# Kernel tuning notes

Hardware: AMD Instinct MI355X
Metric: run time of the kernel (lower is better)

Reference implementation:

```python
import math
import jax, jax.numpy as jnp
import numpy as np

VOCAB = 30522
HIDDEN = 768
TYPE_VOCAB = 2
EPS = 1e-12
MAX_LEN = 5000


def sin_table(dim, max_len=MAX_LEN):
    pos = jnp.arange(max_len, dtype=jnp.float32)[:, None]
    div = jnp.exp(jnp.arange(0, dim, 2, dtype=jnp.float32) * (-(math.log(10000.0) / dim)))
    ang = pos * div  # [max_len, dim//2]
    pe = jnp.zeros((max_len, dim), dtype=jnp.float32)
    pe = pe.at[:, 0::2].set(jnp.sin(ang))
    pe = pe.at[:, 1::2].set(jnp.cos(ang))
    return pe


def setup_inputs() -> dict:
    key = jax.random.key(0)
    k1, k2, k3, k4, k5, k6, k7 = jax.random.split(key, 7)
    B, S = 8, 4096
    input_ids = jax.random.randint(k1, (B, S), 0, VOCAB, dtype=jnp.int64 if jax.config.jax_enable_x64 else jnp.int32)
    tok_struct_vec = jax.random.randint(k2, (B, S, 3), 0, S, dtype=input_ids.dtype)
    sent_struct_vec = jax.random.randint(k3, (B, 64, 2), 0, 64, dtype=input_ids.dtype)
    token_type_ids = jax.random.randint(k4, (B, S), 0, TYPE_VOCAB, dtype=input_ids.dtype)
    word_emb = jax.random.normal(k5, (VOCAB, HIDDEN), dtype=jnp.float32) * 0.02
    word_emb = word_emb.at[0].set(0.0)  # padding_idx=0
    type_emb = jax.random.normal(k6, (TYPE_VOCAB, HIDDEN), dtype=jnp.float32) * 0.02
    ln_w = jnp.ones((HIDDEN,), dtype=jnp.float32)
    ln_b = jnp.zeros((HIDDEN,), dtype=jnp.float32)
    return {"input_ids": input_ids, "tok_struct_vec": tok_struct_vec,
            "sent_struct_vec": sent_struct_vec, "token_type_ids": token_type_ids,
            "word_emb": word_emb, "type_emb": type_emb, "ln_w": ln_w, "ln_b": ln_b}


def reference(input_ids, tok_struct_vec, sent_struct_vec, token_type_ids,
              word_emb, type_emb, ln_w, ln_b):
    B, S = input_ids.shape
    pe = sin_table(HIDDEN)[:S]            # [S, H]
    hs_pe = sin_table(HIDDEN // 3)[:S]    # [S, H/3]

    words = word_emb[input_ids]           # [B,S,H]
    tt = type_emb[token_type_ids]         # [B,S,H]

    # NOTE: faithful to source bug: compute_se closes over para_pos, so all
    # three struct embeddings gather with para_pos (tok_struct_vec[:,:,0]).
    para_pos = tok_struct_vec[:, :, 0]
    g = hs_pe[para_pos]                   # [B,S,H/3]
    struct = jnp.concatenate((g, g, g), axis=2)  # [B,S,H]

    emb = words + pe[None, :, :] + tt + struct
    mu = jnp.mean(emb, axis=-1, keepdims=True)
    var = jnp.mean(jnp.square(emb - mu), axis=-1, keepdims=True)
    out = (emb - mu) / jnp.sqrt(var + EPS) * ln_w + ln_b
    return out  # dropout is identity in eval mode
```

## Files before the change

### kernel.cpp

```cpp
#include <hip/hip_runtime.h>
#include <math.h>

#define HIDDEN 768

#define K768 (-0.011992630692677323f)
#define K256 (-0.035977892078031970f)
#define C256 (0.04641588833612779f)
#define C512 (0.002154434690031884f)

typedef float nfloat4 __attribute__((ext_vector_type(4)));

__global__ __launch_bounds__(256) void emb_ln_kernel(
    const int*   __restrict__ input_ids,
    const int*   __restrict__ tok_struct,
    const int*   __restrict__ token_type,
    const float* __restrict__ word_emb,
    const float* __restrict__ type_emb,
    const float* __restrict__ ln_w,
    const float* __restrict__ ln_b,
    float*       __restrict__ out,
    int S, int BS)
{
    const int wave = threadIdx.x >> 6;
    const int lane = threadIdx.x & 63;
    const int gw   = blockIdx.x * 4 + wave;
    const int NW   = gridDim.x * 4;

    const int h0 = lane * 4;

    const float d0 = __expf((float)h0 * K256);
    const float d1 = __expf((float)(h0 + 2) * K256);
    const float e0 = __expf((float)h0 * K768);
    const float e2 = __expf((float)(h0 + 2) * K768);

    float4 g[3], bb[3], t0[3], t1[3];
    const float4* wv = (const float4*)ln_w;
    const float4* bv = (const float4*)ln_b;
    const float4* te = (const float4*)type_emb;
#pragma unroll
    for (int j = 0; j < 3; ++j) {
        g[j]  = wv[lane + 64 * j];
        bb[j] = bv[lane + 64 * j];
        t0[j] = te[lane + 64 * j];
        t1[j] = te[lane + 64 * j + 192];
    }

    int r = gw;
    if (r >= BS) return;

    int id = input_ids[r];
    int tt = token_type[r];
    int pp = tok_struct[3 * r];
    float4 w[3];
    {
        const float4* wrow = (const float4*)(word_emb + (size_t)id * HIDDEN);
#pragma unroll
        for (int j = 0; j < 3; ++j) w[j] = wrow[lane + 64 * j];
    }

    while (true) {
        const int rn = r + NW;
        const bool has_next = rn < BS;

        int idn = 0, ttn = 0, ppn = 0;
        float4 wn[3];
        if (has_next) {
            idn = input_ids[rn];
            ttn = token_type[rn];
            ppn = tok_struct[3 * rn];
            const float4* wrow = (const float4*)(word_emb + (size_t)idn * HIDDEN);
#pragma unroll
            for (int j = 0; j < 3; ++j) wn[j] = wrow[lane + 64 * j];
        }

        const float fpp = (float)pp;
        float hs[4];
        hs[0] = __sinf(fpp * d0);
        hs[1] = __cosf(fpp * d0);
        hs[2] = __sinf(fpp * d1);
        hs[3] = __cosf(fpp * d1);

        const float fs = (float)(r & (S - 1));

        float v[12];
#pragma unroll
        for (int j = 0; j < 3; ++j) {
            const float scale = (j == 0) ? 1.0f : (j == 1 ? C256 : C512);
            const float a0 = fs * (e0 * scale);
            const float a1 = fs * (e2 * scale);
            const float4 ty = tt ? t1[j] : t0[j];
            v[4 * j + 0] = w[j].x + ty.x + __sinf(a0) + hs[0];
            v[4 * j + 1] = w[j].y + ty.y + __cosf(a0) + hs[1];
            v[4 * j + 2] = w[j].z + ty.z + __sinf(a1) + hs[2];
            v[4 * j + 3] = w[j].w + ty.w + __cosf(a1) + hs[3];
        }

        float s1 = 0.0f, s2 = 0.0f;
#pragma unroll
        for (int i = 0; i < 12; ++i) {
            s1 += v[i];
            s2 = fmaf(v[i], v[i], s2);
        }
#pragma unroll
        for (int off = 1; off < 64; off <<= 1) {
            s1 += __shfl_xor(s1, off, 64);
            s2 += __shfl_xor(s2, off, 64);
        }

        const float inv_n = 1.0f / (float)HIDDEN;
        const float mu = s1 * inv_n;
        const float rstd = rsqrtf(fmaxf(s2 * inv_n - mu * mu, 0.0f) + 1e-12f);

        nfloat4* orow = (nfloat4*)(out + (size_t)r * HIDDEN);
#pragma unroll
        for (int j = 0; j < 3; ++j) {
            nfloat4 rr;
            rr.x = (v[4 * j + 0] - mu) * rstd * g[j].x + bb[j].x;
            rr.y = (v[4 * j + 1] - mu) * rstd * g[j].y + bb[j].y;
            rr.z = (v[4 * j + 2] - mu) * rstd * g[j].z + bb[j].z;
            rr.w = (v[4 * j + 3] - mu) * rstd * g[j].w + bb[j].w;
            __builtin_nontemporal_store(rr, &orow[lane + 64 * j]);
        }

        if (!has_next) break;
        id = idn; tt = ttn; pp = ppn;
        w[0] = wn[0]; w[1] = wn[1]; w[2] = wn[2];
        r = rn;
    }
}

extern "C" void kernel_launch(void* const* d_in, const int* in_sizes, int n_in,
                              void* d_out, int out_size, void* d_ws, size_t ws_size,
                              hipStream_t stream) {
    const int*   input_ids  = (const int*)  d_in[0];
    const int*   tok_struct = (const int*)  d_in[1];
    const int*   token_type = (const int*)  d_in[3];
    const float* word_emb   = (const float*)d_in[4];
    const float* type_emb   = (const float*)d_in[5];
    const float* ln_w       = (const float*)d_in[6];
    const float* ln_b       = (const float*)d_in[7];
    float* out = (float*)d_out;

    const int BS = in_sizes[0];
    const int B  = in_sizes[2] / 128;
    const int S  = BS / B;

    int blocks = 2048;
    if (blocks * 4 > BS) blocks = (BS + 3) / 4;
    emb_ln_kernel<<<blocks, 256, 0, stream>>>(input_ids, tok_struct, token_type,
                                              word_emb, type_emb, ln_w, ln_b,
                                              out, S, BS);
}
```

Measured before the change: 188.5 us.

## Batch four rows per wave with all gathers issued upfront

Each wave now handles a fixed ROWS=4 rows. It first loads all ids and then issues every word-embedding row gather before any compute, instead of running a one-deep software-pipelined grid-stride loop. The type embedding is read from memory per row instead of being held in registers, and launch bounds request 4 blocks per CU. The goal is more memory-level parallelism for the random gathers, paid for with higher register pressure and extra type-embedding loads.

New measurement: 191.1 us. Within noise of the previous version (+1.4%).

```diff
diff --git a/kernel.cpp b/kernel.cpp
--- a/kernel.cpp
+++ b/kernel.cpp
@@ -8,9 +8,11 @@
 #define C256 (0.04641588833612779f)
 #define C512 (0.002154434690031884f)
 
+#define ROWS 4
+
 typedef float nfloat4 __attribute__((ext_vector_type(4)));
 
-__global__ __launch_bounds__(256) void emb_ln_kernel(
+__global__ __launch_bounds__(256, 4) void emb_ln_kernel(
     const int*   __restrict__ input_ids,
     const int*   __restrict__ tok_struct,
     const int*   __restrict__ token_type,
@@ -33,54 +35,53 @@
     const float e0 = __expf((float)h0 * K768);
     const float e2 = __expf((float)(h0 + 2) * K768);
 
-    float4 g[3], bb[3], t0[3], t1[3];
-    const float4* wv = (const float4*)ln_w;
-    const float4* bv = (const float4*)ln_b;
-    const float4* te = (const float4*)type_emb;
+    float4 g[3], bb[3];
+    {
+        const float4* wv = (const float4*)ln_w;
+        const float4* bv = (const float4*)ln_b;
 #pragma unroll
-    for (int j = 0; j < 3; ++j) {
-        g[j]  = wv[lane + 64 * j];
-        bb[j] = bv[lane + 64 * j];
-        t0[j] = te[lane + 64 * j];
-        t1[j] = te[lane + 64 * j + 192];
+        for (int j = 0; j < 3; ++j) {
+            g[j]  = wv[lane + 64 * j];
+            bb[j] = bv[lane + 64 * j];
+        }
     }
 
-    int r = gw;
-    if (r >= BS) return;
+    const int r0 = gw;
+    if (r0 >= BS) return;
 
-    int id = input_ids[r];
-    int tt = token_type[r];
-    int pp = tok_struct[3 * r];
-    float4 w[3];
-    {
-        const float4* wrow = (const float4*)(word_emb + (size_t)id * HIDDEN);
+    int id[ROWS], tt[ROWS], pp[ROWS];
 #pragma unroll
-        for (int j = 0; j < 3; ++j) w[j] = wrow[lane + 64 * j];
+    for (int i = 0; i < ROWS; ++i) {
+        const int rr = r0 + i * NW;
+        const int rc = (rr < BS) ? rr : r0;
+        id[i] = input_ids[rc];
+        tt[i] = token_type[rc];
+        pp[i] = tok_struct[3 * rc];
     }
 
-    while (true) {
-        const int rn = r + NW;
-        const bool has_next = rn < BS;
+    float4 w[ROWS][3];
+#pragma unroll
+    for (int i = 0; i < ROWS; ++i) {
+        const float4* wrow = (const float4*)(word_emb + (size_t)id[i] * HIDDEN);
+#pragma unroll
+        for (int j = 0; j < 3; ++j) w[i][j] = wrow[lane + 64 * j];
+    }
 
-        int idn = 0, ttn = 0, ppn = 0;
-        float4 wn[3];
-        if (has_next) {
-            idn = input_ids[rn];
-            ttn = token_type[rn];
-            ppn = tok_struct[3 * rn];
-            const float4* wrow = (const float4*)(word_emb + (size_t)idn * HIDDEN);
+    const float inv_n = 1.0f / (float)HIDDEN;
+
 #pragma unroll
-            for (int j = 0; j < 3; ++j) wn[j] = wrow[lane + 64 * j];
-        }
+    for (int i = 0; i < ROWS; ++i) {
+        const int r = r0 + i * NW;
+        if (r >= BS) break;
 
-        const float fpp = (float)pp;
-        float hs[4];
-        hs[0] = __sinf(fpp * d0);
-        hs[1] = __cosf(fpp * d0);
-        hs[2] = __sinf(fpp * d1);
-        hs[3] = __cosf(fpp * d1);
+        const float fpp = (float)pp[i];
+        const float hs0 = __sinf(fpp * d0);
+        const float hs1 = __cosf(fpp * d0);
+        const float hs2 = __sinf(fpp * d1);
+        const float hs3 = __cosf(fpp * d1);
 
         const float fs = (float)(r & (S - 1));
+        const float4* ty = (const float4*)(type_emb + tt[i] * HIDDEN);
 
         float v[12];
 #pragma unroll
@@ -88,18 +89,18 @@
             const float scale = (j == 0) ? 1.0f : (j == 1 ? C256 : C512);
             const float a0 = fs * (e0 * scale);
             const float a1 = fs * (e2 * scale);
-            const float4 ty = tt ? t1[j] : t0[j];
-            v[4 * j + 0] = w[j].x + ty.x + __sinf(a0) + hs[0];
-            v[4 * j + 1] = w[j].y + ty.y + __cosf(a0) + hs[1];
-            v[4 * j + 2] = w[j].z + ty.z + __sinf(a1) + hs[2];
-            v[4 * j + 3] = w[j].w + ty.w + __cosf(a1) + hs[3];
+            const float4 t = ty[lane + 64 * j];
+            v[4 * j + 0] = w[i][j].x + t.x + __sinf(a0) + hs0;
+            v[4 * j + 1] = w[i][j].y + t.y + __cosf(a0) + hs1;
+            v[4 * j + 2] = w[i][j].z + t.z + __sinf(a1) + hs2;
+            v[4 * j + 3] = w[i][j].w + t.w + __cosf(a1) + hs3;
         }
 
         float s1 = 0.0f, s2 = 0.0f;
 #pragma unroll
-        for (int i = 0; i < 12; ++i) {
-            s1 += v[i];
-            s2 = fmaf(v[i], v[i], s2);
+        for (int k = 0; k < 12; ++k) {
+            s1 += v[k];
+            s2 = fmaf(v[k], v[k], s2);
         }
 #pragma unroll
         for (int off = 1; off < 64; off <<= 1) {
@@ -107,7 +108,6 @@
             s2 += __shfl_xor(s2, off, 64);
         }
 
-        const float inv_n = 1.0f / (float)HIDDEN;
         const float mu = s1 * inv_n;
         const float rstd = rsqrtf(fmaxf(s2 * inv_n - mu * mu, 0.0f) + 1e-12f);
 
@@ -121,11 +121,6 @@
             rr.w = (v[4 * j + 3] - mu) * rstd * g[j].w + bb[j].w;
             __builtin_nontemporal_store(rr, &orow[lane + 64 * j]);
         }
-
-        if (!has_next) break;
-        id = idn; tt = ttn; pp = ppn;
-        w[0] = wn[0]; w[1] = wn[1]; w[2] = wn[2];
-        r = rn;
     }
 }
 
@@ -145,8 +140,7 @@
     const int B  = in_sizes[2] / 128;
     const int S  = BS / B;
 
-    int blocks = 2048;
-    if (blocks * 4 > BS) blocks = (BS + 3) / 4;
+    int blocks = (BS + 4 * ROWS - 1) / (4 * ROWS);
     emb_ln_kernel<<<blocks, 256, 0, stream>>>(input_ids, tok_struct, token_type,
                                               word_emb, type_emb, ln_w, ln_b,
                                               out, S, BS);
```
